# Kernel tuning notes

Measured on AMD Instinct MI355X. Metric: run time of the kernel, lower is better.

Reference implementation:

```python
import jax, jax.numpy as jnp
import numpy as np

B, H, W = 12, 192, 640
EPS = 1e-7
THRESHOLD = 0.98


def _normalize_flow(f):
    # torch: 2*(f - min)/(max - min) - 1 with GLOBAL min/max
    mn = f.min()
    mx = f.max()
    return 2.0 * (f - mn) / (mx - mn) - 1.0


def setup_inputs() -> dict:
    key = jax.random.key(0)
    ks = jax.random.split(key, 4)
    # optical flow in pixels (up to ~tens of px displacement)
    flow = jax.random.normal(ks[0], (B, 2, H, W), jnp.float32) * 20.0
    depth = jax.random.uniform(ks[1], (B, 1, H, W), jnp.float32, minval=0.1, maxval=10.0)
    # realistic pinhole intrinsics (KITTI-like), padded to 4x4
    Kn = np.eye(4, dtype=np.float32)
    Kn[0, 0] = 0.58 * W
    Kn[1, 1] = 1.92 * H
    Kn[0, 2] = 0.5 * W
    Kn[1, 2] = 0.5 * H
    K = jnp.tile(jnp.asarray(Kn)[None], (B, 1, 1))
    invK = jnp.tile(jnp.asarray(np.linalg.inv(Kn))[None], (B, 1, 1))
    # small-motion camera pose: identity rotation + small translation
    t = jax.random.normal(ks[2], (B, 3), jnp.float32) * 0.05
    pose = jnp.tile(jnp.eye(4, dtype=jnp.float32)[None], (B, 1, 1)).at[:, :3, 3].set(t)
    segmentation = jax.random.randint(ks[3], (B, 1, H, W), 0, 2) > 0
    return {"flow": flow, "depth": depth, "K": K, "invK": invK,
            "pose": pose, "segmentation": segmentation}


def reference(flow, depth, K, invK, pose, segmentation):
    gx = jnp.arange(W, dtype=jnp.float32)
    gy = jnp.arange(H, dtype=jnp.float32)
    grid = jnp.stack(jnp.meshgrid(gx, gy, indexing='xy'), axis=0)  # [2,H,W]

    # ---- compute_dynamic_flow: BackprojectDepth + Project3D + normalize + mask ----
    flow_n = _normalize_flow(flow)
    pix = jnp.concatenate([grid.reshape(2, -1),
                           jnp.ones((1, H * W), jnp.float32)], axis=0)  # [3,HW]
    cam = jnp.einsum('bij,jn->bin', invK[:, :3, :3], pix)               # [B,3,HW]
    cam = depth.reshape(B, 1, -1) * cam
    points = jnp.concatenate([cam, jnp.ones((B, 1, H * W), cam.dtype)], axis=1)  # [B,4,HW]
    P = jnp.matmul(K, pose)[:, :3, :]                                   # [B,3,4]
    cp = jnp.einsum('bij,bjn->bin', P, points)                          # [B,3,HW]
    pix_locs = (cp[:, :2] / (cp[:, 2:3] + EPS)).reshape(B, 2, H, W)
    static_n = _normalize_flow(pix_locs - grid[None])
    dyn = flow_n - static_n
    check = jnp.sqrt(jnp.sum(dyn * dyn, axis=1, keepdims=True))         # [B,1,H,W]
    check = (check - check.min()) / (check.max() - check.min())
    motion_mask = check < THRESHOLD

    coords = jnp.round(grid[None] + flow).astype(jnp.int32)             # [B,2,H,W]
    cxi = jnp.clip(coords[:, 0], 0, W - 1)
    cyi = jnp.clip(coords[:, 1], 0, H - 1)
    idx = (cyi * W + cxi).reshape(B, -1)                                # [B,HW]

    def scat(idx_b, vals_b):  # vals_b: [C,HW] -> scatter columns to idx_b
        return jnp.zeros_like(vals_b).at[:, idx_b].set(vals_b)

    bwd_flow = jax.vmap(scat)(idx, (-flow).reshape(B, 2, -1)).reshape(B, 2, H, W)
    seg_ref = jax.vmap(scat)(idx, segmentation.reshape(B, 1, -1)).reshape(B, 1, H, W)

    return motion_mask, bwd_flow, seg_ref
```

## Files before the change

### kernel.cpp

```cpp
#include <hip/hip_runtime.h>
#include <math.h>

#pragma clang fp contract(off)

namespace {

constexpr int B = 12, H = 192, W = 640;
constexpr int HW  = H * W;
constexpr int BHW = B * HW;
constexpr int NQ  = BHW / 4;
constexpr float EPS = 1e-7f;

constexpr int TA = 256;
constexpr int GA = NQ / TA;

constexpr int TR    = 24;
constexpr int TILES = H / TR;
constexpr int TRW   = TR * W;
constexpr int GW    = B * TILES;
constexpr int GC    = 416;
constexpr int CGRID = GW + GC;
constexpr int TPB   = 1024;


__device__ __forceinline__ void computeP(const float* __restrict__ Kb,
                                         const float* __restrict__ Po, float* P) {
#pragma unroll
    for (int i = 0; i < 3; ++i)
#pragma unroll
        for (int j = 0; j < 4; ++j) {
            float s = Kb[i*4+0] * Po[0*4+j];
            s = s + Kb[i*4+1] * Po[1*4+j];
            s = s + Kb[i*4+2] * Po[2*4+j];
            s = s + Kb[i*4+3] * Po[3*4+j];
            P[i*4+j] = s;
        }
}

__device__ __forceinline__ void static_flow_P(
    const float* __restrict__ iK, const float* __restrict__ P,
    int x, int y, float d, float& sx, float& sy)
{
    float fx = (float)x, fy = (float)y;
    float cam0 = iK[0]*fx + iK[1]*fy + iK[2];
    float cam1 = iK[4]*fx + iK[5]*fy + iK[6];
    float cam2 = iK[8]*fx + iK[9]*fy + iK[10];
    cam0 = d * cam0; cam1 = d * cam1; cam2 = d * cam2;
    float cp0 = P[0]*cam0 + P[1]*cam1 + P[2]*cam2  + P[3];
    float cp1 = P[4]*cam0 + P[5]*cam1 + P[6]*cam2  + P[7];
    float cp2 = P[8]*cam0 + P[9]*cam1 + P[10]*cam2 + P[11];
    float pz = cp2 + EPS;
    sx = cp0 / pz - fx;
    sy = cp1 / pz - fy;
}

__device__ __forceinline__ float norm01(float v, float mn, float mx) {
    return (2.0f * (v - mn)) / (mx - mn) - 1.0f;
}

template<int NW>
__device__ __forceinline__ void blockRed4T(float& a0, float& a1, float& a2, float& a3,
                                           float (*sred)[4], float* bc) {
    for (int off = 32; off; off >>= 1) {
        a0 = fminf(a0, __shfl_down(a0, off, 64));
        a1 = fmaxf(a1, __shfl_down(a1, off, 64));
        a2 = fminf(a2, __shfl_down(a2, off, 64));
        a3 = fmaxf(a3, __shfl_down(a3, off, 64));
    }
    int lane = threadIdx.x & 63, wv = threadIdx.x >> 6;
    if (lane == 0) { sred[wv][0]=a0; sred[wv][1]=a1; sred[wv][2]=a2; sred[wv][3]=a3; }
    __syncthreads();
    if (threadIdx.x == 0) {
#pragma unroll
        for (int w = 1; w < NW; ++w) {
            a0 = fminf(a0, sred[w][0]); a1 = fmaxf(a1, sred[w][1]);
            a2 = fminf(a2, sred[w][2]); a3 = fmaxf(a3, sred[w][3]);
        }
        bc[0]=a0; bc[1]=a1; bc[2]=a2; bc[3]=a3;
    }
    __syncthreads();
    a0=bc[0]; a1=bc[1]; a2=bc[2]; a3=bc[3];
}

template<int NW>
__device__ __forceinline__ void blockRed2T(float& a0, float& a1,
                                           float (*sred)[4], float* bc) {
    for (int off = 32; off; off >>= 1) {
        a0 = fminf(a0, __shfl_down(a0, off, 64));
        a1 = fmaxf(a1, __shfl_down(a1, off, 64));
    }
    int lane = threadIdx.x & 63, wv = threadIdx.x >> 6;
    if (lane == 0) { sred[wv][0]=a0; sred[wv][1]=a1; }
    __syncthreads();
    if (threadIdx.x == 0) {
#pragma unroll
        for (int w = 1; w < NW; ++w) {
            a0 = fminf(a0, sred[w][0]); a1 = fmaxf(a1, sred[w][1]);
        }
        bc[0]=a0; bc[1]=a1;
    }
    __syncthreads();
    a0=bc[0]; a1=bc[1];
}

__global__ void __launch_bounds__(TA)
kA(const float* __restrict__ flow, const float* __restrict__ depth,
   const float* __restrict__ Km, const float* __restrict__ invK,
   const float* __restrict__ pose,
   unsigned int* __restrict__ coords, float* __restrict__ redA)
{
    __shared__ float sred[4][4];
    __shared__ float bc[4];

    int g  = blockIdx.x * TA + threadIdx.x;
    int p0 = g * 4;
    int b  = p0 / HW;
    float P[12];
    computeP(Km + b*16, pose + b*16, P);
    const float* iK = invK + b * 16;
    int n0 = p0 - b * HW;
    int y  = n0 / W;
    int x0 = n0 - y * W;
    float4 fx4 = *(const float4*)(flow + b*2*HW + n0);
    float4 fy4 = *(const float4*)(flow + b*2*HW + HW + n0);
    float4 d4  = *(const float4*)(depth + p0);
    float fmn = fminf(fminf(fx4.x, fx4.y), fminf(fx4.z, fx4.w));
    float fmx = fmaxf(fmaxf(fx4.x, fx4.y), fmaxf(fx4.z, fx4.w));
    fmn = fminf(fmn, fminf(fminf(fy4.x, fy4.y), fminf(fy4.z, fy4.w)));
    fmx = fmaxf(fmx, fmaxf(fmaxf(fy4.x, fy4.y), fmaxf(fy4.z, fy4.w)));
    float smn = INFINITY, smx = -INFINITY;
    float fxa[4] = {fx4.x, fx4.y, fx4.z, fx4.w};
    float fya[4] = {fy4.x, fy4.y, fy4.z, fy4.w};
    float da[4]  = {d4.x, d4.y, d4.z, d4.w};
    uint4 cc;
    unsigned* cca = (unsigned*)&cc;
#pragma unroll
    for (int j = 0; j < 4; ++j) {
        float sx, sy;
        static_flow_P(iK, P, x0 + j, y, da[j], sx, sy);
        smn = fminf(smn, fminf(sx, sy));
        smx = fmaxf(smx, fmaxf(sx, sy));
        int cxi = (int)rintf((float)(x0 + j) + fxa[j]);
        int cyi = (int)rintf((float)y + fya[j]);
        cxi = min(max(cxi, 0), W - 1);
        cyi = min(max(cyi, 0), H - 1);
        cca[j] = ((unsigned)cyi << 10) | (unsigned)cxi;
    }
    *(uint4*)(coords + p0) = cc;

    blockRed4T<4>(fmn, fmx, smn, smx, sred, bc);
    if (threadIdx.x == 0) {
        redA[blockIdx.x*4+0] = fmn; redA[blockIdx.x*4+1] = fmx;
        redA[blockIdx.x*4+2] = smn; redA[blockIdx.x*4+3] = smx;
    }
}

__global__ void __launch_bounds__(TPB)
kBW(const float* __restrict__ flow, const float* __restrict__ depth,
    const float* __restrict__ Km, const float* __restrict__ invK,
    const float* __restrict__ pose, const int* __restrict__ seg,
    const unsigned int* __restrict__ coords,
    const float* __restrict__ redA, float* __restrict__ redB,
    float* __restrict__ out)
{
    __shared__ unsigned int smem[TRW];
    if (blockIdx.x < GW) {
        const int b    = blockIdx.x / TILES;
        const int tile = blockIdx.x - b * TILES;
        const unsigned t0 = (unsigned)(tile * TR);

        for (int q = threadIdx.x; q < TRW/4; q += TPB)
            *(uint4*)(smem + q*4) = make_uint4(0u,0u,0u,0u);
        __syncthreads();

        const uint4* cb = (const uint4*)(coords + b * HW);
        for (int q = threadIdx.x; q < HW / 4; q += TPB) {
            uint4 c4 = cb[q];
            unsigned ca[4] = {c4.x, c4.y, c4.z, c4.w};
            int n0 = q * 4;
#pragma unroll
            for (int j = 0; j < 4; ++j) {
                unsigned r = (ca[j] >> 10) - t0;
                if (r < (unsigned)TR)
                    atomicMax(&smem[r * W + (ca[j] & 1023u)],
                              (unsigned)(n0 + j + 1));
            }
        }
        __syncthreads();

        const float* fb = flow + b * 2 * HW;
        const int*   sb = seg + b * HW;
        const int    nbase = (int)t0 * W;
        for (int q = threadIdx.x; q < TRW/4; q += TPB) {
            uint4 w4 = *(const uint4*)(smem + q*4);
            unsigned wa[4] = {w4.x, w4.y, w4.z, w4.w};
            float4 bx4, by4, sg4;
            float* bxa = (float*)&bx4;
            float* bya = (float*)&by4;
            float* sga = (float*)&sg4;
#pragma unroll
            for (int j = 0; j < 4; ++j) {
                float bx = 0.0f, by = 0.0f, sg = 0.0f;
                if (wa[j]) {
                    int nw = (int)wa[j] - 1;
                    bx = -fb[nw];
                    by = -fb[HW + nw];
                    sg = sb[nw] ? 1.0f : 0.0f;
                }
                bxa[j] = bx; bya[j] = by; sga[j] = sg;
            }
            int n = nbase + q * 4;
            *(float4*)(out + BHW + b*2*HW + n)      = bx4;
            *(float4*)(out + BHW + b*2*HW + HW + n) = by4;
            *(float4*)(out + 3*BHW + b*HW + n)      = sg4;
        }
        return;
    }

    float (*sred)[4] = (float(*)[4])smem;
    float* bc = (float*)(smem + 64);

    float gfmn = INFINITY, gfmx = -INFINITY, gsmn = INFINITY, gsmx = -INFINITY;
    for (int i = threadIdx.x; i < GA; i += TPB) {
        gfmn = fminf(gfmn, redA[i*4+0]); gfmx = fmaxf(gfmx, redA[i*4+1]);
        gsmn = fminf(gsmn, redA[i*4+2]); gsmx = fmaxf(gsmx, redA[i*4+3]);
    }
    blockRed4T<16>(gfmn, gfmx, gsmn, gsmx, sred, bc);

    float cmn = INFINITY, cmx = -INFINITY;
    float P[12]; int bCur = -1;
    const int cb = blockIdx.x - GW;
    const int stride = GC * TPB;
    for (int g = cb * TPB + threadIdx.x; g < NQ; g += stride) {
        int p0 = g * 4;
        int b  = p0 / HW;
        if (b != bCur) { computeP(Km + b*16, pose + b*16, P); bCur = b; }
        const float* iK = invK + b * 16;
        int n0 = p0 - b * HW;
        int y  = n0 / W;
        int x0 = n0 - y * W;
        float4 fx4 = *(const float4*)(flow + b*2*HW + n0);
        float4 fy4 = *(const float4*)(flow + b*2*HW + HW + n0);
        float4 d4  = *(const float4*)(depth + p0);
        float fxa[4] = {fx4.x, fx4.y, fx4.z, fx4.w};
        float fya[4] = {fy4.x, fy4.y, fy4.z, fy4.w};
        float da[4]  = {d4.x, d4.y, d4.z, d4.w};
        float4 cv;
        float* cva = (float*)&cv;
#pragma unroll
        for (int j = 0; j < 4; ++j) {
            float sx, sy;
            static_flow_P(iK, P, x0 + j, y, da[j], sx, sy);
            float dx = norm01(fxa[j], gfmn, gfmx) - norm01(sx, gsmn, gsmx);
            float dy = norm01(fya[j], gfmn, gfmx) - norm01(sy, gsmn, gsmx);
            float c = sqrtf(dx*dx + dy*dy);
            cva[j] = c;
            cmn = fminf(cmn, c); cmx = fmaxf(cmx, c);
        }
        *(float4*)(out + p0) = cv;
    }
    blockRed2T<16>(cmn, cmx, sred, bc);
    if (threadIdx.x == 0) { redB[cb*2] = cmn; redB[cb*2+1] = cmx; }
}

__global__ void __launch_bounds__(TA)
kM(const float* __restrict__ redB, float* __restrict__ out)
{
    __shared__ float sred[4][4];
    __shared__ float bc[4];

    float gcmn = INFINITY, gcmx = -INFINITY;
    for (int i = threadIdx.x; i < GC; i += TA) {
        gcmn = fminf(gcmn, redB[2*i]); gcmx = fmaxf(gcmx, redB[2*i+1]);
    }
    blockRed2T<4>(gcmn, gcmx, sred, bc);

    int p0 = (blockIdx.x * TA + threadIdx.x) * 4;
    float4 c4 = *(const float4*)(out + p0);
    float ca[4] = {c4.x, c4.y, c4.z, c4.w};
    float4 m4;
    float* ma = (float*)&m4;
#pragma unroll
    for (int j = 0; j < 4; ++j) {
        float cn = (ca[j] - gcmn) / (gcmx - gcmn);
        ma[j] = (cn < 0.98f) ? 1.0f : 0.0f;
    }
    *(float4*)(out + p0) = m4;
}

}

extern "C" void kernel_launch(void* const* d_in, const int* in_sizes, int n_in,
                              void* d_out, int out_size, void* d_ws, size_t ws_size,
                              hipStream_t stream) {
    const float* flow  = (const float*)d_in[0];
    const float* depth = (const float*)d_in[1];
    const float* Km    = (const float*)d_in[2];
    const float* invK  = (const float*)d_in[3];
    const float* pose  = (const float*)d_in[4];
    const int*   seg   = (const int*)d_in[5];
    float* out = (float*)d_out;

    float* redA = (float*)d_ws;
    float* redB = (float*)((char*)d_ws + 24576);
    unsigned int* coords = (unsigned int*)((char*)d_ws + 32768);

    kA <<<GA,    TA,  0, stream>>>(flow, depth, Km, invK, pose, coords, redA);
    kBW<<<CGRID, TPB, 0, stream>>>(flow, depth, Km, invK, pose, seg, coords,
                                   redA, redB, out);
    kM <<<GA,    TA,  0, stream>>>(redB, out);
}
```

Before: 142.5 us.

## Bucket scatter targets by row tile so each scatter block reads only its entries

The first kernel now bins each source pixel's destination into per-batch, per-row-tile buckets. It uses shared-memory atomic counters and then reserves space in a global counter array, which a new tiny kernel zeroes. The scatter blocks now read only the entries of their own bucket instead of scanning the whole batch's coordinate array, and the tile height drops from 24 to 6 rows to give more blocks. This removes the redundant reads of the full coordinate array by every tile. In exchange it adds atomics and non-coalesced bucket writes in the first kernel, an extra launch, and a much larger bucket workspace of B*TILES*HW entries.

```diff
diff --git a/kernel.cpp b/kernel.cpp
--- a/kernel.cpp
+++ b/kernel.cpp
@@ -11,13 +11,15 @@
 constexpr int NQ  = BHW / 4;
 constexpr float EPS = 1e-7f;
 
-constexpr int TA = 256;
-constexpr int GA = NQ / TA;
-
-constexpr int TR    = 24;
+constexpr int TA  = 256;
+constexpr int GA  = NQ / TA;
+constexpr int BPB = (HW / 4) / TA;
+
+constexpr int TR    = 6;
 constexpr int TILES = H / TR;
 constexpr int TRW   = TR * W;
-constexpr int GW    = B * TILES;
+constexpr int NBK   = B * TILES;
+constexpr int GW    = NBK;
 constexpr int GC    = 416;
 constexpr int CGRID = GW + GC;
 constexpr int TPB   = 1024;
@@ -103,14 +105,24 @@
     a0=bc[0]; a1=bc[1];
 }
 
+__global__ void kZ(unsigned* __restrict__ cnt) {
+    cnt[threadIdx.x] = 0u;
+}
+
 __global__ void __launch_bounds__(TA)
 kA(const float* __restrict__ flow, const float* __restrict__ depth,
    const float* __restrict__ Km, const float* __restrict__ invK,
    const float* __restrict__ pose,
-   unsigned int* __restrict__ coords, float* __restrict__ redA)
+   unsigned* __restrict__ cnt, unsigned* __restrict__ bkt,
+   float* __restrict__ redA)
 {
     __shared__ float sred[4][4];
     __shared__ float bc[4];
+    __shared__ unsigned tcnt[TILES];
+    __shared__ unsigned tbase[TILES];
+
+    if (threadIdx.x < TILES) tcnt[threadIdx.x] = 0u;
+    __syncthreads();
 
     int g  = blockIdx.x * TA + threadIdx.x;
     int p0 = g * 4;
@@ -132,8 +144,8 @@
     float fxa[4] = {fx4.x, fx4.y, fx4.z, fx4.w};
     float fya[4] = {fy4.x, fy4.y, fy4.z, fy4.w};
     float da[4]  = {d4.x, d4.y, d4.z, d4.w};
-    uint4 cc;
-    unsigned* cca = (unsigned*)&cc;
+    int      t_j[4];
+    unsigned off_j[4], e_j[4];
 #pragma unroll
     for (int j = 0; j < 4; ++j) {
         float sx, sy;
@@ -144,9 +156,22 @@
         int cyi = (int)rintf((float)y + fya[j]);
         cxi = min(max(cxi, 0), W - 1);
         cyi = min(max(cyi, 0), H - 1);
-        cca[j] = ((unsigned)cyi << 10) | (unsigned)cxi;
-    }
-    *(uint4*)(coords + p0) = cc;
+        int t   = cyi / TR;
+        int pos = (cyi - t * TR) * W + cxi;
+        t_j[j]   = t;
+        e_j[j]   = ((unsigned)(n0 + j) << 12) | (unsigned)pos;
+        off_j[j] = atomicAdd(&tcnt[t], 1u);
+    }
+    __syncthreads();
+    if (threadIdx.x < TILES)
+        tbase[threadIdx.x] =
+            atomicAdd(&cnt[b * TILES + threadIdx.x], tcnt[threadIdx.x]);
+    __syncthreads();
+#pragma unroll
+    for (int j = 0; j < 4; ++j) {
+        int idx = (b * TILES + t_j[j]) * HW + (int)(tbase[t_j[j]] + off_j[j]);
+        bkt[idx] = e_j[j];
+    }
 
     blockRed4T<4>(fmn, fmx, smn, smx, sred, bc);
     if (threadIdx.x == 0) {
@@ -159,38 +184,29 @@
 kBW(const float* __restrict__ flow, const float* __restrict__ depth,
     const float* __restrict__ Km, const float* __restrict__ invK,
     const float* __restrict__ pose, const int* __restrict__ seg,
-    const unsigned int* __restrict__ coords,
+    const unsigned* __restrict__ cnt, const unsigned* __restrict__ bkt,
     const float* __restrict__ redA, float* __restrict__ redB,
     float* __restrict__ out)
 {
-    __shared__ unsigned int smem[TRW];
+    __shared__ unsigned smem[TRW];
     if (blockIdx.x < GW) {
-        const int b    = blockIdx.x / TILES;
-        const int tile = blockIdx.x - b * TILES;
-        const unsigned t0 = (unsigned)(tile * TR);
-
-        for (int q = threadIdx.x; q < TRW/4; q += TPB)
-            *(uint4*)(smem + q*4) = make_uint4(0u,0u,0u,0u);
+        const int wb = blockIdx.x;
+        const int b  = wb / TILES;
+        const int t  = wb - b * TILES;
+        for (int i = threadIdx.x; i < TRW; i += TPB) smem[i] = 0u;
         __syncthreads();
 
-        const uint4* cb = (const uint4*)(coords + b * HW);
-        for (int q = threadIdx.x; q < HW / 4; q += TPB) {
-            uint4 c4 = cb[q];
-            unsigned ca[4] = {c4.x, c4.y, c4.z, c4.w};
-            int n0 = q * 4;
-#pragma unroll
-            for (int j = 0; j < 4; ++j) {
-                unsigned r = (ca[j] >> 10) - t0;
-                if (r < (unsigned)TR)
-                    atomicMax(&smem[r * W + (ca[j] & 1023u)],
-                              (unsigned)(n0 + j + 1));
-            }
+        const unsigned count = cnt[wb];
+        const unsigned* src = bkt + wb * HW;
+        for (unsigned i = threadIdx.x; i < count; i += TPB) {
+            unsigned e = src[i];
+            atomicMax(&smem[e & 4095u], (e >> 12) + 1u);
         }
         __syncthreads();
 
         const float* fb = flow + b * 2 * HW;
         const int*   sb = seg + b * HW;
-        const int    nbase = (int)t0 * W;
+        const int    nbase = t * TRW;
         for (int q = threadIdx.x; q < TRW/4; q += TPB) {
             uint4 w4 = *(const uint4*)(smem + q*4);
             unsigned wa[4] = {w4.x, w4.y, w4.z, w4.w};
@@ -301,12 +317,14 @@
     const int*   seg   = (const int*)d_in[5];
     float* out = (float*)d_out;
 
-    float* redA = (float*)d_ws;
-    float* redB = (float*)((char*)d_ws + 24576);
-    unsigned int* coords = (unsigned int*)((char*)d_ws + 32768);
-
-    kA <<<GA,    TA,  0, stream>>>(flow, depth, Km, invK, pose, coords, redA);
-    kBW<<<CGRID, TPB, 0, stream>>>(flow, depth, Km, invK, pose, seg, coords,
+    unsigned* cnt  = (unsigned*)d_ws;
+    float*    redA = (float*)((char*)d_ws + 4096);
+    float*    redB = (float*)((char*)d_ws + 28672);
+    unsigned* bkt  = (unsigned*)((char*)d_ws + 32768);
+
+    kZ <<<1,     NBK, 0, stream>>>(cnt);
+    kA <<<GA,    TA,  0, stream>>>(flow, depth, Km, invK, pose, cnt, bkt, redA);
+    kBW<<<CGRID, TPB, 0, stream>>>(flow, depth, Km, invK, pose, seg, cnt, bkt,
                                    redA, redB, out);
     kM <<<GA,    TA,  0, stream>>>(redB, out);
 }
```

Measured after the change: 137.4 us. 3.6% less time.
